# Performance work log

Hardware: AMD Instinct MI355X
Metric: run time of the kernel (lower is better)

Reference implementation:

```python
import jax, jax.numpy as jnp
import numpy as np

B, S, H, F, E, K = 2, 1024, 1024, 4096, 8, 2
TOPK_RATIO = 0.55
EPS = 1e-8


def _ste(x, q):
    # straight-through estimator: forward = q, backward = identity on x
    return x + jax.lax.stop_gradient(q - x)


def ternary_weight(w):
    # BitNet b1.58 absmean ternarization: W -> clip(round(W/mean|W|), -1, 1) * mean|W|
    s = jnp.maximum(jnp.mean(jnp.abs(w)), EPS)
    q = jnp.clip(jnp.round(w / s), -1.0, 1.0) * s
    return _ste(w, q)


def quant_act_int4(x):
    # per-token symmetric int4 fake-quant (range [-7, 7]) with STE
    s = jnp.maximum(jnp.max(jnp.abs(x), axis=-1, keepdims=True), EPS) / 7.0
    q = jnp.clip(jnp.round(x / s), -7.0, 7.0) * s
    return _ste(x, q)


def quant_act_topk_int8(x, ratio):
    # keep top ceil(ratio*d) values by magnitude per token, then int8 fake-quant
    d = x.shape[-1]
    k = int(np.ceil(ratio * d))
    thresh = jax.lax.top_k(jnp.abs(x), k)[0][..., -1:]
    xm = jnp.where(jnp.abs(x) >= thresh, x, 0.0)
    s = jnp.maximum(jnp.max(jnp.abs(xm), axis=-1, keepdims=True), EPS) / 127.0
    q = jnp.clip(jnp.round(xm / s), -127.0, 127.0) * s
    return _ste(xm, q)


def quant_weight_int8(w):
    # per-tensor absmax int8 fake-quant for the router (Int8Linear) with STE
    s = jnp.maximum(jnp.max(jnp.abs(w)), EPS) / 127.0
    q = jnp.clip(jnp.round(w / s), -127.0, 127.0) * s
    return _ste(w, q)


def setup_inputs() -> dict:
    key = jax.random.key(0)
    ks = jax.random.split(key, 5)
    x = jax.random.normal(ks[0], (B, S, H), jnp.float32)
    w_gate = jax.random.normal(ks[1], (E, F, H), jnp.float32) * 0.02
    w_up = jax.random.normal(ks[2], (E, F, H), jnp.float32) * 0.02
    w_down = jax.random.normal(ks[3], (E, H, F), jnp.float32) * 0.02
    w_router = jax.random.normal(ks[4], (E, H), jnp.float32) * 0.02
    return {"x": x, "w_gate": w_gate, "w_up": w_up, "w_down": w_down, "w_router": w_router}


def reference(x, w_gate, w_up, w_down, w_router):
    T = B * S
    xf = x.reshape(T, H)

    # --- router (Int8Linear, higher precision than ternary) ---
    logits = xf @ quant_weight_int8(w_router).T          # [T, E]
    probs = jax.nn.softmax(logits, axis=-1)
    gates, idx = jax.lax.top_k(probs, K)                  # [T, K]
    gates = gates / jnp.sum(gates, axis=-1, keepdims=True)
    # dense combine weights [T, E]
    comb = jnp.zeros((T, E), x.dtype).at[jnp.arange(T)[:, None], idx].set(gates)

    # --- experts: BitFFN (SwiGLU with ternary weights + quantized activations) ---
    xq = quant_act_int4(xf)                               # shared int4 input quant

    def expert(wg, wu, wd):
        g = xq @ ternary_weight(wg).T                     # [T, F]
        u = xq @ ternary_weight(wu).T                     # [T, F]
        h = jax.nn.silu(g) * u
        hq = quant_act_topk_int8(h, TOPK_RATIO)
        return hq @ ternary_weight(wd).T                  # [T, H]

    expert_out = jax.vmap(expert)(w_gate, w_up, w_down)   # [E, T, H]
    out = jnp.einsum('te,eth->th', comb, expert_out)      # gated combine
    return out.reshape(B, S, H)
```

## Files before the change

### kernel.cpp

```cpp
#include <hip/hip_runtime.h>
#include <cstdint>
#include <cstddef>


#define T_TOK 2048
#define HDIM  1024
#define FDIM  4096
#define NEXP  8
#define FH    (FDIM * HDIM)
#define KTOP  2253
#define EPSF  1e-8f

typedef int v4i  __attribute__((ext_vector_type(4)));
typedef int v16i __attribute__((ext_vector_type(16)));

__global__ __launch_bounds__(256) void k_wabs_partial(const float* __restrict__ wg,
                                                      const float* __restrict__ wu,
                                                      const float* __restrict__ wd,
                                                      float* __restrict__ partials) {
  int m = blockIdx.x, blk = blockIdx.y, tid = threadIdx.x;
  const float* base = (m < 8) ? (wg + (size_t)m * FH)
                    : (m < 16) ? (wu + (size_t)(m - 8) * FH)
                               : (wd + (size_t)(m - 16) * FH);
  size_t start = (size_t)blk * 65536;
  float s = 0.f;
#pragma unroll 4
  for (int i = 0; i < 64; i++) {
    float4 v = *(const float4*)(base + start + (size_t)i * 1024 + tid * 4);
    s += fabsf(v.x) + fabsf(v.y) + fabsf(v.z) + fabsf(v.w);
  }
  for (int o = 32; o > 0; o >>= 1) s += __shfl_down(s, o);
  __shared__ float lds[4];
  if ((tid & 63) == 0) lds[tid >> 6] = s;
  __syncthreads();
  if (tid == 0) partials[m * 64 + blk] = lds[0] + lds[1] + lds[2] + lds[3];
}

__global__ __launch_bounds__(256) void k_scales(const float* __restrict__ wr,
                                                const float* __restrict__ partials,
                                                float* __restrict__ s_w,
                                                float* __restrict__ wrq) {
  int tid = threadIdx.x;
  __shared__ float lds[4];
  __shared__ float sbc;
  for (int m = 0; m < 24; m++) {
    float v = 0.f;
    if (tid < 64) v = partials[m * 64 + tid];
    for (int o = 32; o > 0; o >>= 1) v += __shfl_down(v, o);
    if ((tid & 63) == 0) lds[tid >> 6] = v;
    __syncthreads();
    if (tid == 0) s_w[m] = fmaxf((lds[0] + lds[1] + lds[2] + lds[3]) / (float)FH, EPSF);
    __syncthreads();
  }
  float mx = 0.f;
  for (int i = tid; i < NEXP * HDIM; i += 256) mx = fmaxf(mx, fabsf(wr[i]));
  for (int o = 32; o > 0; o >>= 1) mx = fmaxf(mx, __shfl_down(mx, o));
  if ((tid & 63) == 0) lds[tid >> 6] = mx;
  __syncthreads();
  if (tid == 0)
    sbc = fmaxf(fmaxf(fmaxf(lds[0], lds[1]), fmaxf(lds[2], lds[3])), EPSF) / 127.0f;
  __syncthreads();
  float s = sbc;
  for (int i = tid; i < NEXP * HDIM; i += 256) {
    float q = fminf(fmaxf(rintf(wr[i] / s), -127.f), 127.f);
    wrq[i] = q * s;
  }
}

__global__ __launch_bounds__(256) void k_quant_w(const float* __restrict__ w,
                                                 signed char* __restrict__ q,
                                                 const float* __restrict__ scales) {
  const size_t total16 = (size_t)NEXP * FH / 16;
  for (size_t i16 = (size_t)blockIdx.x * 256 + threadIdx.x; i16 < total16;
       i16 += (size_t)gridDim.x * 256) {
    int e = (int)(i16 >> 18);
    float s = scales[e];
    const float4* src = (const float4*)(w + i16 * 16);
    signed char outb[16];
#pragma unroll
    for (int j = 0; j < 4; j++) {
      float4 v = src[j];
      outb[j * 4 + 0] = (signed char)(int)fminf(fmaxf(rintf(v.x / s), -1.f), 1.f);
      outb[j * 4 + 1] = (signed char)(int)fminf(fmaxf(rintf(v.y / s), -1.f), 1.f);
      outb[j * 4 + 2] = (signed char)(int)fminf(fmaxf(rintf(v.z / s), -1.f), 1.f);
      outb[j * 4 + 3] = (signed char)(int)fminf(fmaxf(rintf(v.w / s), -1.f), 1.f);
    }
    *(int4*)(q + i16 * 16) = *(const int4*)outb;
  }
}

__global__ __launch_bounds__(256) void k_act_router(const float* __restrict__ x,
                                                    const float* __restrict__ wrq,
                                                    signed char* __restrict__ xq,
                                                    float* __restrict__ sx,
                                                    int* __restrict__ tok_e,
                                                    float* __restrict__ tok_g,
                                                    int* __restrict__ cnt) {
  int t = blockIdx.x, tid = threadIdx.x;
  float4 xv = *(const float4*)(x + (size_t)t * HDIM + tid * 4);
  __shared__ float lds[4];
  __shared__ float sbc;
  __shared__ float part[8][256];
  __shared__ float lg[8];
  float mx = fmaxf(fmaxf(fabsf(xv.x), fabsf(xv.y)), fmaxf(fabsf(xv.z), fabsf(xv.w)));
  for (int o = 32; o > 0; o >>= 1) mx = fmaxf(mx, __shfl_down(mx, o));
  if ((tid & 63) == 0) lds[tid >> 6] = mx;
  __syncthreads();
  if (tid == 0)
    sbc = fmaxf(fmaxf(fmaxf(lds[0], lds[1]), fmaxf(lds[2], lds[3])), EPSF) / 7.0f;
  __syncthreads();
  float s = sbc;
  int q0 = (int)fminf(fmaxf(rintf(xv.x / s), -7.f), 7.f);
  int q1 = (int)fminf(fmaxf(rintf(xv.y / s), -7.f), 7.f);
  int q2 = (int)fminf(fmaxf(rintf(xv.z / s), -7.f), 7.f);
  int q3 = (int)fminf(fmaxf(rintf(xv.w / s), -7.f), 7.f);
  int packed = (q0 & 255) | ((q1 & 255) << 8) | ((q2 & 255) << 16) | (q3 << 24);
  *(int*)(xq + (size_t)t * HDIM + tid * 4) = packed;
  if (tid == 0) sx[t] = s;
#pragma unroll
  for (int e = 0; e < 8; e++) {
    float4 w = *(const float4*)(wrq + e * HDIM + tid * 4);
    part[e][tid] = xv.x * w.x + xv.y * w.y + xv.z * w.z + xv.w * w.w;
  }
  __syncthreads();
  if (tid < 8) {
    float sum = 0.f;
    for (int i = 0; i < 256; i++) sum += part[tid][i];
    lg[tid] = sum;
  }
  __syncthreads();
  if (tid == 0) {
    float m = lg[0];
    for (int e = 1; e < 8; e++) m = fmaxf(m, lg[e]);
    float p[8]; float S = 0.f;
    for (int e = 0; e < 8; e++) { p[e] = expf(lg[e] - m); S += p[e]; }
    for (int e = 0; e < 8; e++) p[e] /= S;
    int e0 = 0;
    for (int e = 1; e < 8; e++) if (p[e] > p[e0]) e0 = e;
    int e1 = -1;
    for (int e = 0; e < 8; e++) { if (e == e0) continue; if (e1 < 0 || p[e] > p[e1]) e1 = e; }
    float g0 = p[e0], g1 = p[e1], gs = g0 + g1;
    tok_e[2 * t] = e0;  tok_e[2 * t + 1] = e1;
    tok_g[2 * t] = g0 / gs;  tok_g[2 * t + 1] = g1 / gs;
    atomicAdd(&cnt[e0], 1); atomicAdd(&cnt[e1], 1);
  }
}

__global__ void k_plan(const int* __restrict__ cnt, int* __restrict__ offs,
                       int* __restrict__ tile_e, int* __restrict__ tile_m0,
                       int* __restrict__ tile_cnt) {
  if (threadIdx.x == 0 && blockIdx.x == 0) {
    int o = 0;
    for (int e = 0; e < 8; e++) { offs[e] = o; o += cnt[e]; }
    offs[8] = o;
    int tt = 0;
    for (int e = 0; e < 8; e++)
      for (int m0 = 0; m0 < cnt[e]; m0 += 64) { tile_e[tt] = e; tile_m0[tt] = m0; tt++; }
    *tile_cnt = tt;
  }
}

__global__ __launch_bounds__(256) void k_scatter(const int* __restrict__ tok_e,
                                                 const float* __restrict__ tok_g,
                                                 const float* __restrict__ sx,
                                                 const int* __restrict__ offs,
                                                 int* __restrict__ cnt2,
                                                 int* __restrict__ pair_tok,
                                                 float* __restrict__ pair_gate,
                                                 float* __restrict__ pair_sx) {
  int t = blockIdx.x * 256 + threadIdx.x;
  if (t >= T_TOK) return;
  for (int k = 0; k < 2; k++) {
    int e = tok_e[2 * t + k];
    int pos = offs[e] + atomicAdd(&cnt2[e], 1);
    pair_tok[pos] = t;
    pair_gate[pos] = tok_g[2 * t + k];
    pair_sx[pos] = sx[t];
  }
}

__global__ __launch_bounds__(256) void k_gemm_gu(const signed char* __restrict__ xq,
                                                 const signed char* __restrict__ wgq,
                                                 const signed char* __restrict__ wuq,
                                                 const int* __restrict__ tile_e,
                                                 const int* __restrict__ tile_m0,
                                                 const int* __restrict__ tile_cnt,
                                                 const int* __restrict__ cnt,
                                                 const int* __restrict__ offs,
                                                 const int* __restrict__ pair_tok,
                                                 const float* __restrict__ pair_sx,
                                                 const float* __restrict__ s_w,
                                                 float* __restrict__ hbuf) {
  int bx = blockIdx.x;
  if (bx >= *tile_cnt) return;
  int e = tile_e[bx], m0 = tile_m0[bx];
  int cnt_e = cnt[e], pbase = offs[e];
  int tid = threadIdx.x;
  int wave = tid >> 6, lane = tid & 63, ln = lane & 31, kh = lane >> 5;
  int r0 = m0 + ln, r1 = m0 + 32 + ln;
  int tok0 = pair_tok[pbase + ((r0 < cnt_e) ? r0 : cnt_e - 1)];
  int tok1 = pair_tok[pbase + ((r1 < cnt_e) ? r1 : cnt_e - 1)];
  const signed char* ap0 = xq + (size_t)tok0 * HDIM + kh * 16;
  const signed char* ap1 = xq + (size_t)tok1 * HDIM + kh * 16;
  int fbase = blockIdx.y * 128 + wave * 32;
  const signed char* bg = wgq + (size_t)e * FH + (size_t)(fbase + ln) * HDIM + kh * 16;
  const signed char* bu = wuq + (size_t)e * FH + (size_t)(fbase + ln) * HDIM + kh * 16;
  v16i accg0 = {0}, accg1 = {0}, accu0 = {0}, accu1 = {0};
#pragma unroll 4
  for (int k0 = 0; k0 < HDIM; k0 += 32) {
    v4i a0 = *(const v4i*)(ap0 + k0);
    v4i a1 = *(const v4i*)(ap1 + k0);
    v4i b0 = *(const v4i*)(bg + k0);
    v4i b1 = *(const v4i*)(bu + k0);
    accg0 = __builtin_amdgcn_mfma_i32_32x32x32_i8(a0, b0, accg0, 0, 0, 0);
    accg1 = __builtin_amdgcn_mfma_i32_32x32x32_i8(a1, b0, accg1, 0, 0, 0);
    accu0 = __builtin_amdgcn_mfma_i32_32x32x32_i8(a0, b1, accu0, 0, 0, 0);
    accu1 = __builtin_amdgcn_mfma_i32_32x32x32_i8(a1, b1, accu1, 0, 0, 0);
  }
  float sg = s_w[e], su = s_w[8 + e];
#pragma unroll
  for (int r = 0; r < 16; r++) {
    int rr = (r & 3) + 8 * (r >> 2) + 4 * kh;
#pragma unroll
    for (int mt = 0; mt < 2; mt++) {
      int ml = m0 + mt * 32 + rr;
      if (ml < cnt_e) {
        int p = pbase + ml;
        float sxv = pair_sx[p];
        int gi = (mt == 0) ? accg0[r] : accg1[r];
        int ui = (mt == 0) ? accu0[r] : accu1[r];
        float gf = (float)gi * (sxv * sg);
        float uf = (float)ui * (sxv * su);
        float h = gf / (1.0f + expf(-gf)) * uf;
        hbuf[(size_t)p * FDIM + fbase + ln] = h;
      }
    }
  }
}

__global__ __launch_bounds__(256) void k_select(const float* __restrict__ hbuf,
                                                signed char* __restrict__ hq,
                                                const float* __restrict__ pair_gate,
                                                float* __restrict__ pair_f) {
  int p = blockIdx.x, tid = threadIdx.x;
  const float* row = hbuf + (size_t)p * FDIM;
  float vals[16];
  unsigned int ua[16];
  float mx = 0.f;
#pragma unroll
  for (int j = 0; j < 16; j++) {
    float v = row[tid + j * 256];
    vals[j] = v;
    unsigned int u = __float_as_uint(v) & 0x7fffffffu;
    ua[j] = u;
    mx = fmaxf(mx, __uint_as_float(u));
  }
  __shared__ float lds[4];
  __shared__ float smax;
  __shared__ unsigned int hist[256];
  __shared__ unsigned int S[256];
  __shared__ unsigned int prefix_s;
  __shared__ int need_s;
  for (int o = 32; o > 0; o >>= 1) mx = fmaxf(mx, __shfl_down(mx, o));
  if ((tid & 63) == 0) lds[tid >> 6] = mx;
  __syncthreads();
  if (tid == 0) {
    smax = fmaxf(fmaxf(lds[0], lds[1]), fmaxf(lds[2], lds[3]));
    prefix_s = 0u;
    need_s = KTOP;
  }
  __syncthreads();
  for (int pass = 3; pass >= 0; pass--) {
    hist[tid] = 0u;
    __syncthreads();
    unsigned int pref = prefix_s;
    int shift = pass * 8;
#pragma unroll
    for (int j = 0; j < 16; j++) {
      unsigned int u = ua[j];
      bool in = (pass == 3) || ((u >> (shift + 8)) == (pref >> (shift + 8)));
      if (in) atomicAdd(&hist[(u >> shift) & 255], 1u);
    }
    __syncthreads();
    S[tid] = hist[tid];
    __syncthreads();
    for (int off = 1; off < 256; off <<= 1) {
      unsigned int v = (tid + off < 256) ? S[tid + off] : 0u;
      __syncthreads();
      S[tid] += v;
      __syncthreads();
    }
    int need = need_s;
    unsigned int above = (tid < 255) ? S[tid + 1] : 0u;
    if ((int)S[tid] >= need && (int)above < need) {
      need_s = need - (int)above;
      prefix_s = prefix_s | ((unsigned int)tid << shift);
    }
    __syncthreads();
  }
  unsigned int thr_bits = prefix_s;
  float sq = fmaxf(smax, EPSF) / 127.0f;
#pragma unroll
  for (int j = 0; j < 16; j++) {
    float m = (ua[j] >= thr_bits) ? vals[j] : 0.0f;
    float q = fminf(fmaxf(rintf(m / sq), -127.f), 127.f);
    hq[(size_t)p * FDIM + tid + j * 256] = (signed char)(int)q;
  }
  if (tid == 0) pair_f[p] = pair_gate[p] * sq;
}

__global__ __launch_bounds__(256) void k_gemm_down(const signed char* __restrict__ hq,
                                                   const signed char* __restrict__ wdq,
                                                   const int* __restrict__ tile_e,
                                                   const int* __restrict__ tile_m0,
                                                   const int* __restrict__ tile_cnt,
                                                   const int* __restrict__ cnt,
                                                   const int* __restrict__ offs,
                                                   const int* __restrict__ pair_tok,
                                                   const float* __restrict__ pair_f,
                                                   const float* __restrict__ s_w,
                                                   float* __restrict__ out) {
  int bx = blockIdx.x;
  if (bx >= *tile_cnt) return;
  int e = tile_e[bx], m0 = tile_m0[bx];
  int cnt_e = cnt[e], pbase = offs[e];
  int tid = threadIdx.x;
  int wave = tid >> 6, lane = tid & 63, ln = lane & 31, kh = lane >> 5;
  int r0 = m0 + ln, r1 = m0 + 32 + ln;
  int p0 = pbase + ((r0 < cnt_e) ? r0 : cnt_e - 1);
  int p1 = pbase + ((r1 < cnt_e) ? r1 : cnt_e - 1);
  const signed char* ap0 = hq + (size_t)p0 * FDIM + kh * 16;
  const signed char* ap1 = hq + (size_t)p1 * FDIM + kh * 16;
  int nbase = blockIdx.y * 128 + wave * 32;
  const signed char* bp = wdq + (size_t)e * FH + (size_t)(nbase + ln) * FDIM + kh * 16;
  v16i acc0 = {0}, acc1 = {0};
#pragma unroll 4
  for (int k0 = 0; k0 < FDIM; k0 += 32) {
    v4i a0 = *(const v4i*)(ap0 + k0);
    v4i a1 = *(const v4i*)(ap1 + k0);
    v4i b = *(const v4i*)(bp + k0);
    acc0 = __builtin_amdgcn_mfma_i32_32x32x32_i8(a0, b, acc0, 0, 0, 0);
    acc1 = __builtin_amdgcn_mfma_i32_32x32x32_i8(a1, b, acc1, 0, 0, 0);
  }
  float sd = s_w[16 + e];
  int col = nbase + ln;
#pragma unroll
  for (int r = 0; r < 16; r++) {
    int rr = (r & 3) + 8 * (r >> 2) + 4 * kh;
#pragma unroll
    for (int mt = 0; mt < 2; mt++) {
      int ml = m0 + mt * 32 + rr;
      if (ml < cnt_e) {
        int p = pbase + ml;
        int ai = (mt == 0) ? acc0[r] : acc1[r];
        float v = (float)ai * (pair_f[p] * sd);
        atomicAdd(out + (size_t)pair_tok[p] * HDIM + col, v);
      }
    }
  }
}

extern "C" void kernel_launch(void* const* d_in, const int* in_sizes, int n_in,
                              void* d_out, int out_size, void* d_ws, size_t ws_size,
                              hipStream_t stream) {
  const float* x  = (const float*)d_in[0];
  const float* wg = (const float*)d_in[1];
  const float* wu = (const float*)d_in[2];
  const float* wd = (const float*)d_in[3];
  const float* wr = (const float*)d_in[4];
  float* out = (float*)d_out;
  char* ws = (char*)d_ws;
  (void)in_sizes; (void)n_in; (void)out_size; (void)ws_size;

  size_t o = 0;
  auto alloc = [&](size_t b) { size_t r = o; o += (b + 255) & ~(size_t)255; return r; };
  float* partials   = (float*)(ws + alloc(24 * 64 * 4));
  float* s_w        = (float*)(ws + alloc(24 * 4));
  float* wrq        = (float*)(ws + alloc((size_t)NEXP * HDIM * 4));
  int*   tok_e      = (int*)  (ws + alloc((size_t)T_TOK * 2 * 4));
  float* tok_g      = (float*)(ws + alloc((size_t)T_TOK * 2 * 4));
  int*   cnt        = (int*)  (ws + alloc(256));
  int*   cnt2       = cnt + 8;
  int*   offs       = (int*)  (ws + alloc(16 * 4));
  int*   tile_e     = (int*)  (ws + alloc(128 * 4));
  int*   tile_m0    = (int*)  (ws + alloc(128 * 4));
  int*   tile_cnt   = (int*)  (ws + alloc(4));
  int*   pair_tok   = (int*)  (ws + alloc(4096 * 4));
  float* pair_gate  = (float*)(ws + alloc(4096 * 4));
  float* pair_sx    = (float*)(ws + alloc(4096 * 4));
  float* pair_f     = (float*)(ws + alloc(4096 * 4));
  float* sx         = (float*)(ws + alloc((size_t)T_TOK * 4));
  signed char* xq   = (signed char*)(ws + alloc((size_t)T_TOK * HDIM));
  signed char* wgq  = (signed char*)(ws + alloc((size_t)NEXP * FH));
  signed char* wuq  = (signed char*)(ws + alloc((size_t)NEXP * FH));
  signed char* wdq  = (signed char*)(ws + alloc((size_t)NEXP * FH));
  float* hbuf       = (float*)(ws + alloc((size_t)4096 * FDIM * 4));
  signed char* hq   = (signed char*)(ws + alloc((size_t)4096 * FDIM));

  hipMemsetAsync(cnt, 0, 64, stream);
  hipMemsetAsync(out, 0, (size_t)T_TOK * HDIM * 4, stream);

  k_wabs_partial<<<dim3(24, 64), 256, 0, stream>>>(wg, wu, wd, partials);
  k_scales<<<1, 256, 0, stream>>>(wr, partials, s_w, wrq);
  k_quant_w<<<4096, 256, 0, stream>>>(wg, wgq, s_w);
  k_quant_w<<<4096, 256, 0, stream>>>(wu, wuq, s_w + 8);
  k_quant_w<<<4096, 256, 0, stream>>>(wd, wdq, s_w + 16);
  k_act_router<<<T_TOK, 256, 0, stream>>>(x, wrq, xq, sx, tok_e, tok_g, cnt);
  k_plan<<<1, 64, 0, stream>>>(cnt, offs, tile_e, tile_m0, tile_cnt);
  k_scatter<<<8, 256, 0, stream>>>(tok_e, tok_g, sx, offs, cnt2, pair_tok, pair_gate, pair_sx);
  k_gemm_gu<<<dim3(72, 32), 256, 0, stream>>>(xq, wgq, wuq, tile_e, tile_m0, tile_cnt,
                                              cnt, offs, pair_tok, pair_sx, s_w, hbuf);
  k_select<<<4096, 256, 0, stream>>>(hbuf, hq, pair_gate, pair_f);
  k_gemm_down<<<dim3(72, 8), 256, 0, stream>>>(hq, wdq, tile_e, tile_m0, tile_cnt,
                                               cnt, offs, pair_tok, pair_f, s_w, out);
}
```

Before: 962.5 us.

## Pre-pack weights and activations into MFMA fragment layout, store h as fp16

```diff
diff --git a/kernel.cpp b/kernel.cpp
--- a/kernel.cpp
+++ b/kernel.cpp
@@ -10,6 +10,7 @@
 #define FH    (FDIM * HDIM)
 #define KTOP  2253
 #define EPSF  1e-8f
+#define PPAD  4608
 
 typedef int v4i  __attribute__((ext_vector_type(4)));
 typedef int v16i __attribute__((ext_vector_type(16)));
@@ -67,26 +68,28 @@
   }
 }
 
-__global__ __launch_bounds__(256) void k_quant_w(const float* __restrict__ w,
-                                                 signed char* __restrict__ q,
-                                                 const float* __restrict__ scales) {
-  const size_t total16 = (size_t)NEXP * FH / 16;
-  for (size_t i16 = (size_t)blockIdx.x * 256 + threadIdx.x; i16 < total16;
-       i16 += (size_t)gridDim.x * 256) {
-    int e = (int)(i16 >> 18);
-    float s = scales[e];
-    const float4* src = (const float4*)(w + i16 * 16);
-    signed char outb[16];
-#pragma unroll
-    for (int j = 0; j < 4; j++) {
-      float4 v = src[j];
-      outb[j * 4 + 0] = (signed char)(int)fminf(fmaxf(rintf(v.x / s), -1.f), 1.f);
-      outb[j * 4 + 1] = (signed char)(int)fminf(fmaxf(rintf(v.y / s), -1.f), 1.f);
-      outb[j * 4 + 2] = (signed char)(int)fminf(fmaxf(rintf(v.z / s), -1.f), 1.f);
-      outb[j * 4 + 3] = (signed char)(int)fminf(fmaxf(rintf(v.w / s), -1.f), 1.f);
-    }
-    *(int4*)(q + i16 * 16) = *(const int4*)outb;
-  }
+template <int KD, int RD>
+__global__ __launch_bounds__(256) void k_quant_pack(const float* __restrict__ w,
+                                                    signed char* __restrict__ q,
+                                                    const float* __restrict__ scales) {
+  constexpr int CCH = KD / 32, GR = RD / 32;
+  int idx = blockIdx.x * 256 + threadIdx.x;
+  int l = idx & 63;
+  int c = (idx >> 6) % CCH;
+  int g = (idx / (64 * CCH)) % GR;
+  int e = idx / (64 * CCH * GR);
+  const float* src = w + ((size_t)e * RD + g * 32 + (l & 31)) * KD + c * 32 + (l >> 5) * 16;
+  float s = scales[e];
+  signed char outb[16];
+#pragma unroll
+  for (int j = 0; j < 4; j++) {
+    float4 v = *(const float4*)(src + j * 4);
+    outb[j * 4 + 0] = (signed char)(int)fminf(fmaxf(rintf(v.x / s), -1.f), 1.f);
+    outb[j * 4 + 1] = (signed char)(int)fminf(fmaxf(rintf(v.y / s), -1.f), 1.f);
+    outb[j * 4 + 2] = (signed char)(int)fminf(fmaxf(rintf(v.z / s), -1.f), 1.f);
+    outb[j * 4 + 3] = (signed char)(int)fminf(fmaxf(rintf(v.w / s), -1.f), 1.f);
+  }
+  *(int4*)(q + (size_t)idx * 16) = *(const int4*)outb;
 }
 
 __global__ __launch_bounds__(256) void k_act_router(const float* __restrict__ x,
@@ -151,7 +154,7 @@
                        int* __restrict__ tile_cnt) {
   if (threadIdx.x == 0 && blockIdx.x == 0) {
     int o = 0;
-    for (int e = 0; e < 8; e++) { offs[e] = o; o += cnt[e]; }
+    for (int e = 0; e < 8; e++) { offs[e] = o; o += (cnt[e] + 63) & ~63; }
     offs[8] = o;
     int tt = 0;
     for (int e = 0; e < 8; e++)
@@ -179,45 +182,52 @@
   }
 }
 
-__global__ __launch_bounds__(256) void k_gemm_gu(const signed char* __restrict__ xq,
-                                                 const signed char* __restrict__ wgq,
-                                                 const signed char* __restrict__ wuq,
+__global__ __launch_bounds__(256) void k_packA(const int* __restrict__ pair_tok,
+                                               const signed char* __restrict__ xq,
+                                               signed char* __restrict__ xqp) {
+  int idx = blockIdx.x * 256 + threadIdx.x;
+  int l = idx & 63, c = (idx >> 6) & 31, pgrp = idx >> 11;
+  int p = pgrp * 32 + (l & 31);
+  int tok = pair_tok[p];
+  const signed char* src = xq + (size_t)tok * HDIM + c * 32 + (l >> 5) * 16;
+  *(int4*)(xqp + (size_t)idx * 16) = *(const int4*)src;
+}
+
+__global__ __launch_bounds__(256) void k_gemm_gu(const signed char* __restrict__ xqp,
+                                                 const signed char* __restrict__ wgp,
+                                                 const signed char* __restrict__ wup,
                                                  const int* __restrict__ tile_e,
                                                  const int* __restrict__ tile_m0,
                                                  const int* __restrict__ tile_cnt,
                                                  const int* __restrict__ cnt,
                                                  const int* __restrict__ offs,
-                                                 const int* __restrict__ pair_tok,
                                                  const float* __restrict__ pair_sx,
                                                  const float* __restrict__ s_w,
-                                                 float* __restrict__ hbuf) {
+                                                 unsigned short* __restrict__ hbuf) {
   int bx = blockIdx.x;
   if (bx >= *tile_cnt) return;
   int e = tile_e[bx], m0 = tile_m0[bx];
   int cnt_e = cnt[e], pbase = offs[e];
   int tid = threadIdx.x;
   int wave = tid >> 6, lane = tid & 63, ln = lane & 31, kh = lane >> 5;
-  int r0 = m0 + ln, r1 = m0 + 32 + ln;
-  int tok0 = pair_tok[pbase + ((r0 < cnt_e) ? r0 : cnt_e - 1)];
-  int tok1 = pair_tok[pbase + ((r1 < cnt_e) ? r1 : cnt_e - 1)];
-  const signed char* ap0 = xq + (size_t)tok0 * HDIM + kh * 16;
-  const signed char* ap1 = xq + (size_t)tok1 * HDIM + kh * 16;
-  int fbase = blockIdx.y * 128 + wave * 32;
-  const signed char* bg = wgq + (size_t)e * FH + (size_t)(fbase + ln) * HDIM + kh * 16;
-  const signed char* bu = wuq + (size_t)e * FH + (size_t)(fbase + ln) * HDIM + kh * 16;
+  int fgrp = blockIdx.y * 4 + wave;
+  const signed char* bg = wgp + (((size_t)e * 128 + fgrp) * 32) * 1024 + lane * 16;
+  const signed char* bu = wup + (((size_t)e * 128 + fgrp) * 32) * 1024 + lane * 16;
+  const signed char* ap = xqp + ((size_t)((pbase + m0) >> 5) * 32) * 1024 + lane * 16;
   v16i accg0 = {0}, accg1 = {0}, accu0 = {0}, accu1 = {0};
-#pragma unroll 4
-  for (int k0 = 0; k0 < HDIM; k0 += 32) {
-    v4i a0 = *(const v4i*)(ap0 + k0);
-    v4i a1 = *(const v4i*)(ap1 + k0);
-    v4i b0 = *(const v4i*)(bg + k0);
-    v4i b1 = *(const v4i*)(bu + k0);
+#pragma unroll 8
+  for (int c = 0; c < 32; c++) {
+    v4i a0 = *(const v4i*)(ap + c * 1024);
+    v4i a1 = *(const v4i*)(ap + 32768 + c * 1024);
+    v4i b0 = *(const v4i*)(bg + c * 1024);
+    v4i b1 = *(const v4i*)(bu + c * 1024);
     accg0 = __builtin_amdgcn_mfma_i32_32x32x32_i8(a0, b0, accg0, 0, 0, 0);
     accg1 = __builtin_amdgcn_mfma_i32_32x32x32_i8(a1, b0, accg1, 0, 0, 0);
     accu0 = __builtin_amdgcn_mfma_i32_32x32x32_i8(a0, b1, accu0, 0, 0, 0);
     accu1 = __builtin_amdgcn_mfma_i32_32x32x32_i8(a1, b1, accu1, 0, 0, 0);
   }
   float sg = s_w[e], su = s_w[8 + e];
+  int col = blockIdx.y * 128 + wave * 32 + ln;
 #pragma unroll
   for (int r = 0; r < 16; r++) {
     int rr = (r & 3) + 8 * (r >> 2) + 4 * kh;
@@ -232,85 +242,71 @@
         float gf = (float)gi * (sxv * sg);
         float uf = (float)ui * (sxv * su);
         float h = gf / (1.0f + expf(-gf)) * uf;
-        hbuf[(size_t)p * FDIM + fbase + ln] = h;
+        ((_Float16*)hbuf)[(size_t)p * FDIM + col] = (_Float16)h;
       }
     }
   }
 }
 
-__global__ __launch_bounds__(256) void k_select(const float* __restrict__ hbuf,
-                                                signed char* __restrict__ hq,
+__global__ __launch_bounds__(256) void k_select(const unsigned short* __restrict__ hbuf,
+                                                signed char* __restrict__ hqp,
                                                 const float* __restrict__ pair_gate,
                                                 float* __restrict__ pair_f) {
-  int p = blockIdx.x, tid = threadIdx.x;
-  const float* row = hbuf + (size_t)p * FDIM;
-  float vals[16];
-  unsigned int ua[16];
-  float mx = 0.f;
-#pragma unroll
-  for (int j = 0; j < 16; j++) {
-    float v = row[tid + j * 256];
-    vals[j] = v;
+  int wv = threadIdx.x >> 6, lane = threadIdx.x & 63;
+  int p = blockIdx.x * 4 + wv;
+  const unsigned short* row = hbuf + (size_t)p * FDIM + lane * 64;
+  unsigned short hs[64];
+#pragma unroll
+  for (int i = 0; i < 8; i++)
+    *(uint4*)(hs + i * 8) = *(const uint4*)(row + i * 8);
+  unsigned int ua[64];
+  unsigned int mxb = 0;
+#pragma unroll
+  for (int j = 0; j < 64; j++) {
+    float v = (float)(((const _Float16*)hs)[j]);
     unsigned int u = __float_as_uint(v) & 0x7fffffffu;
     ua[j] = u;
-    mx = fmaxf(mx, __uint_as_float(u));
-  }
-  __shared__ float lds[4];
-  __shared__ float smax;
-  __shared__ unsigned int hist[256];
-  __shared__ unsigned int S[256];
-  __shared__ unsigned int prefix_s;
-  __shared__ int need_s;
-  for (int o = 32; o > 0; o >>= 1) mx = fmaxf(mx, __shfl_down(mx, o));
-  if ((tid & 63) == 0) lds[tid >> 6] = mx;
-  __syncthreads();
-  if (tid == 0) {
-    smax = fmaxf(fmaxf(lds[0], lds[1]), fmaxf(lds[2], lds[3]));
-    prefix_s = 0u;
-    need_s = KTOP;
-  }
-  __syncthreads();
-  for (int pass = 3; pass >= 0; pass--) {
-    hist[tid] = 0u;
-    __syncthreads();
-    unsigned int pref = prefix_s;
-    int shift = pass * 8;
-#pragma unroll
-    for (int j = 0; j < 16; j++) {
-      unsigned int u = ua[j];
-      bool in = (pass == 3) || ((u >> (shift + 8)) == (pref >> (shift + 8)));
-      if (in) atomicAdd(&hist[(u >> shift) & 255], 1u);
+    mxb = (u > mxb) ? u : mxb;
+  }
+  for (int o = 32; o > 0; o >>= 1) {
+    unsigned int t = (unsigned int)__shfl_down((int)mxb, o);
+    mxb = (t > mxb) ? t : mxb;
+  }
+  mxb = (unsigned int)__shfl((int)mxb, 0);
+  unsigned int lo = 0, hi = 0x80000000u;
+  for (int it = 0; it < 31; ++it) {
+    unsigned int mid = (lo + hi) >> 1;
+    int cnt = 0;
+#pragma unroll
+    for (int j = 0; j < 64; j++)
+      cnt += (int)__popcll(__ballot(ua[j] >= mid));
+    if (cnt >= KTOP) lo = mid; else hi = mid;
+  }
+  unsigned int thr = lo;
+  float smax = fmaxf(__uint_as_float(mxb), EPSF);
+  float sq = smax / 127.0f;
+  int pgrp = p >> 5, ln = p & 31;
+#pragma unroll
+  for (int gj = 0; gj < 4; gj++) {
+    int c = 2 * lane + (gj >> 1);
+    int kh = gj & 1;
+    signed char outb[16];
+#pragma unroll
+    for (int t = 0; t < 16; t++) {
+      int j = gj * 16 + t;
+      float v = (float)(((const _Float16*)hs)[j]);
+      float m = (ua[j] >= thr) ? v : 0.0f;
+      float q = fminf(fmaxf(rintf(m / sq), -127.f), 127.f);
+      outb[t] = (signed char)(int)q;
     }
-    __syncthreads();
-    S[tid] = hist[tid];
-    __syncthreads();
-    for (int off = 1; off < 256; off <<= 1) {
-      unsigned int v = (tid + off < 256) ? S[tid + off] : 0u;
-      __syncthreads();
-      S[tid] += v;
-      __syncthreads();
-    }
-    int need = need_s;
-    unsigned int above = (tid < 255) ? S[tid + 1] : 0u;
-    if ((int)S[tid] >= need && (int)above < need) {
-      need_s = need - (int)above;
-      prefix_s = prefix_s | ((unsigned int)tid << shift);
-    }
-    __syncthreads();
-  }
-  unsigned int thr_bits = prefix_s;
-  float sq = fmaxf(smax, EPSF) / 127.0f;
-#pragma unroll
-  for (int j = 0; j < 16; j++) {
-    float m = (ua[j] >= thr_bits) ? vals[j] : 0.0f;
-    float q = fminf(fmaxf(rintf(m / sq), -127.f), 127.f);
-    hq[(size_t)p * FDIM + tid + j * 256] = (signed char)(int)q;
-  }
-  if (tid == 0) pair_f[p] = pair_gate[p] * sq;
-}
-
-__global__ __launch_bounds__(256) void k_gemm_down(const signed char* __restrict__ hq,
-                                                   const signed char* __restrict__ wdq,
+    *(int4*)(hqp + ((size_t)((size_t)pgrp * 128 + c) * 64 + kh * 32 + ln) * 16) =
+        *(const int4*)outb;
+  }
+  if (lane == 0) pair_f[p] = pair_gate[p] * sq;
+}
+
+__global__ __launch_bounds__(256) void k_gemm_down(const signed char* __restrict__ hqp,
+                                                   const signed char* __restrict__ wdp,
                                                    const int* __restrict__ tile_e,
                                                    const int* __restrict__ tile_m0,
                                                    const int* __restrict__ tile_cnt,
@@ -326,24 +322,20 @@
   int cnt_e = cnt[e], pbase = offs[e];
   int tid = threadIdx.x;
   int wave = tid >> 6, lane = tid & 63, ln = lane & 31, kh = lane >> 5;
-  int r0 = m0 + ln, r1 = m0 + 32 + ln;
-  int p0 = pbase + ((r0 < cnt_e) ? r0 : cnt_e - 1);
-  int p1 = pbase + ((r1 < cnt_e) ? r1 : cnt_e - 1);
-  const signed char* ap0 = hq + (size_t)p0 * FDIM + kh * 16;
-  const signed char* ap1 = hq + (size_t)p1 * FDIM + kh * 16;
-  int nbase = blockIdx.y * 128 + wave * 32;
-  const signed char* bp = wdq + (size_t)e * FH + (size_t)(nbase + ln) * FDIM + kh * 16;
+  int grp_n = blockIdx.y * 4 + wave;
+  const signed char* bp = wdp + (((size_t)e * 32 + grp_n) * 128) * 1024 + lane * 16;
+  const signed char* ap = hqp + ((size_t)((pbase + m0) >> 5) * 128) * 1024 + lane * 16;
   v16i acc0 = {0}, acc1 = {0};
-#pragma unroll 4
-  for (int k0 = 0; k0 < FDIM; k0 += 32) {
-    v4i a0 = *(const v4i*)(ap0 + k0);
-    v4i a1 = *(const v4i*)(ap1 + k0);
-    v4i b = *(const v4i*)(bp + k0);
+#pragma unroll 8
+  for (int c = 0; c < 128; c++) {
+    v4i a0 = *(const v4i*)(ap + (size_t)c * 1024);
+    v4i a1 = *(const v4i*)(ap + 131072 + (size_t)c * 1024);
+    v4i b  = *(const v4i*)(bp + (size_t)c * 1024);
     acc0 = __builtin_amdgcn_mfma_i32_32x32x32_i8(a0, b, acc0, 0, 0, 0);
     acc1 = __builtin_amdgcn_mfma_i32_32x32x32_i8(a1, b, acc1, 0, 0, 0);
   }
   float sd = s_w[16 + e];
-  int col = nbase + ln;
+  int col = blockIdx.y * 128 + wave * 32 + ln;
 #pragma unroll
   for (int r = 0; r < 16; r++) {
     int rr = (r & 3) + 8 * (r >> 2) + 4 * kh;
@@ -385,32 +377,35 @@
   int*   tile_e     = (int*)  (ws + alloc(128 * 4));
   int*   tile_m0    = (int*)  (ws + alloc(128 * 4));
   int*   tile_cnt   = (int*)  (ws + alloc(4));
-  int*   pair_tok   = (int*)  (ws + alloc(4096 * 4));
-  float* pair_gate  = (float*)(ws + alloc(4096 * 4));
-  float* pair_sx    = (float*)(ws + alloc(4096 * 4));
-  float* pair_f     = (float*)(ws + alloc(4096 * 4));
+  int*   pair_tok   = (int*)  (ws + alloc((size_t)PPAD * 4));
+  float* pair_gate  = (float*)(ws + alloc((size_t)PPAD * 4));
+  float* pair_sx    = (float*)(ws + alloc((size_t)PPAD * 4));
+  float* pair_f     = (float*)(ws + alloc((size_t)PPAD * 4));
   float* sx         = (float*)(ws + alloc((size_t)T_TOK * 4));
   signed char* xq   = (signed char*)(ws + alloc((size_t)T_TOK * HDIM));
-  signed char* wgq  = (signed char*)(ws + alloc((size_t)NEXP * FH));
-  signed char* wuq  = (signed char*)(ws + alloc((size_t)NEXP * FH));
-  signed char* wdq  = (signed char*)(ws + alloc((size_t)NEXP * FH));
-  float* hbuf       = (float*)(ws + alloc((size_t)4096 * FDIM * 4));
-  signed char* hq   = (signed char*)(ws + alloc((size_t)4096 * FDIM));
+  signed char* xqp  = (signed char*)(ws + alloc((size_t)PPAD * HDIM));
+  signed char* wgp  = (signed char*)(ws + alloc((size_t)NEXP * FH));
+  signed char* wup  = (signed char*)(ws + alloc((size_t)NEXP * FH));
+  signed char* wdp  = (signed char*)(ws + alloc((size_t)NEXP * FH));
+  unsigned short* hbuf = (unsigned short*)(ws + alloc((size_t)PPAD * FDIM * 2));
+  signed char* hqp  = (signed char*)(ws + alloc((size_t)PPAD * FDIM));
 
   hipMemsetAsync(cnt, 0, 64, stream);
+  hipMemsetAsync(pair_tok, 0, (size_t)PPAD * 4, stream);
   hipMemsetAsync(out, 0, (size_t)T_TOK * HDIM * 4, stream);
 
   k_wabs_partial<<<dim3(24, 64), 256, 0, stream>>>(wg, wu, wd, partials);
   k_scales<<<1, 256, 0, stream>>>(wr, partials, s_w, wrq);
-  k_quant_w<<<4096, 256, 0, stream>>>(wg, wgq, s_w);
-  k_quant_w<<<4096, 256, 0, stream>>>(wu, wuq, s_w + 8);
-  k_quant_w<<<4096, 256, 0, stream>>>(wd, wdq, s_w + 16);
+  k_quant_pack<1024, 4096><<<8192, 256, 0, stream>>>(wg, wgp, s_w);
+  k_quant_pack<1024, 4096><<<8192, 256, 0, stream>>>(wu, wup, s_w + 8);
+  k_quant_pack<4096, 1024><<<8192, 256, 0, stream>>>(wd, wdp, s_w + 16);
   k_act_router<<<T_TOK, 256, 0, stream>>>(x, wrq, xq, sx, tok_e, tok_g, cnt);
   k_plan<<<1, 64, 0, stream>>>(cnt, offs, tile_e, tile_m0, tile_cnt);
   k_scatter<<<8, 256, 0, stream>>>(tok_e, tok_g, sx, offs, cnt2, pair_tok, pair_gate, pair_sx);
-  k_gemm_gu<<<dim3(72, 32), 256, 0, stream>>>(xq, wgq, wuq, tile_e, tile_m0, tile_cnt,
-                                              cnt, offs, pair_tok, pair_sx, s_w, hbuf);
-  k_select<<<4096, 256, 0, stream>>>(hbuf, hq, pair_gate, pair_f);
-  k_gemm_down<<<dim3(72, 8), 256, 0, stream>>>(hq, wdq, tile_e, tile_m0, tile_cnt,
+  k_packA<<<PPAD / 4, 256, 0, stream>>>(pair_tok, xq, xqp);
+  k_gemm_gu<<<dim3(72, 32), 256, 0, stream>>>(xqp, wgp, wup, tile_e, tile_m0, tile_cnt,
+                                              cnt, offs, pair_sx, s_w, hbuf);
+  k_select<<<PPAD / 4, 256, 0, stream>>>(hbuf, hqp, pair_gate, pair_f);
+  k_gemm_down<<<dim3(72, 8), 256, 0, stream>>>(hqp, wdp, tile_e, tile_m0, tile_cnt,
                                                cnt, offs, pair_tok, pair_f, s_w, out);
 }
```

After: 816.6 us. 15.2% less time.
